# Performance work log

Hardware: AMD Instinct MI355X
Metric: run time of the kernel (lower is better)

## Reference

```python
import jax, jax.numpy as jnp
import numpy as np

NUM_GRAPHS = 128


def _gcn_layer(x, W, b, src, dst, out_norm, in_norm, n_nodes):
    # DGL GraphConv, norm='both': x * outdeg^{-1/2}, sum-aggregate src->dst, * indeg^{-1/2}, then @W + b
    x = x * out_norm[:, None]
    agg = jax.ops.segment_sum(x[src], dst, num_segments=n_nodes)  # [N, d]
    agg = agg * in_norm[:, None]
    return agg @ W + b


def setup_inputs() -> dict:
    key = jax.random.key(0)
    ks = jax.random.split(key, 10)
    N, E, D, H, P, C = 100000, 1600000, 128, 128, 64, 10
    h = jax.random.normal(ks[0], (N, D), dtype=jnp.float32)
    perm_features = jax.random.normal(ks[1], (NUM_GRAPHS, P), dtype=jnp.float32)
    W1 = jax.random.normal(ks[2], (D, H), dtype=jnp.float32) * (1.0 / np.sqrt(D))
    b1 = jnp.zeros((H,), dtype=jnp.float32)
    W2 = jax.random.normal(ks[3], (H, H), dtype=jnp.float32) * (1.0 / np.sqrt(H))
    b2 = jnp.zeros((H,), dtype=jnp.float32)
    Wc = jax.random.normal(ks[4], (H + P, C), dtype=jnp.float32) * (1.0 / np.sqrt(H + P))
    bc = jnp.zeros((C,), dtype=jnp.float32)
    src = jax.random.randint(ks[5], (E,), 0, N, dtype=jnp.int64)
    dst = jax.random.randint(ks[6], (E,), 0, N, dtype=jnp.int64)
    graph_ids = jnp.sort(jax.random.randint(ks[7], (N,), 0, NUM_GRAPHS, dtype=jnp.int64))
    return {"h": h, "perm_features": perm_features, "W1": W1, "b1": b1,
            "W2": W2, "b2": b2, "Wc": Wc, "bc": bc,
            "src": src, "dst": dst, "graph_ids": graph_ids}


def reference(h, perm_features, W1, b1, W2, b2, Wc, bc, src, dst, graph_ids):
    N = h.shape[0]
    ones_e = jnp.ones(src.shape[0], dtype=h.dtype)
    out_deg = jnp.maximum(jax.ops.segment_sum(ones_e, src, num_segments=N), 1.0)
    in_deg = jnp.maximum(jax.ops.segment_sum(ones_e, dst, num_segments=N), 1.0)
    out_norm = jax.lax.rsqrt(out_deg)
    in_norm = jax.lax.rsqrt(in_deg)

    x = _gcn_layer(h, W1, b1, src, dst, out_norm, in_norm, N)
    x = jax.nn.relu(x)
    x = _gcn_layer(x, W2, b2, src, dst, out_norm, in_norm, N)

    # dgl.mean_nodes: per-graph mean of node features
    sums = jax.ops.segment_sum(x, graph_ids, num_segments=NUM_GRAPHS)  # [G, H]
    counts = jnp.maximum(
        jax.ops.segment_sum(jnp.ones(N, dtype=x.dtype), graph_ids, num_segments=NUM_GRAPHS), 1.0)
    hg = sums / counts[:, None]

    combined = jnp.concatenate([hg, perm_features], axis=1)  # [G, H+P]
    return combined @ Wc + bc
```

## Files before the change

kernel.cpp:

```cpp
#include <hip/hip_runtime.h>


#define NUM_G 128
#define PB_EDGES 4096
#define W_BIN 128

typedef unsigned int uint32;
typedef short bf16x8 __attribute__((ext_vector_type(8)));
typedef float f32x4 __attribute__((ext_vector_type(4)));

__device__ __forceinline__ float bflo(uint32 u) { return __uint_as_float(u << 16); }
__device__ __forceinline__ float bfhi(uint32 u) { return __uint_as_float(u & 0xffff0000u); }
__device__ __forceinline__ uint32 f2bf_bits(float f) {
    uint32 b = __float_as_uint(f);
    return (b + 0x7fffu + ((b >> 16) & 1u)) >> 16;
}
__device__ __forceinline__ uint32 pack2(float a, float b) {
    return f2bf_bits(a) | (f2bf_bits(b) << 16);
}

__global__ __launch_bounds__(256) void p1_hist(const int* __restrict__ src,
                                               const int* __restrict__ dst, int E,
                                               int NBIN, int B, int* __restrict__ bh) {
    __shared__ int hist[1024];
    int b = blockIdx.x;
    int pipe = (b >= B) ? 1 : 0;
    int bb = pipe ? b - B : b;
    const int* key = pipe ? src : dst;
    for (int i = threadIdx.x; i < NBIN; i += 256) hist[i] = 0;
    __syncthreads();
    int base = bb * PB_EDGES;
    for (int c = threadIdx.x; c < PB_EDGES / 4; c += 256) {
        int e = base + c * 4;
        if (e + 3 < E) {
            int4 k4 = *(const int4*)(key + e);
            atomicAdd(&hist[k4.x >> 7], 1);
            atomicAdd(&hist[k4.y >> 7], 1);
            atomicAdd(&hist[k4.z >> 7], 1);
            atomicAdd(&hist[k4.w >> 7], 1);
        } else {
            for (int i = e; i < E && i < e + 4; i++) atomicAdd(&hist[key[i] >> 7], 1);
        }
    }
    __syncthreads();
    int* outp = bh + (size_t)pipe * NBIN * B;
    for (int k = threadIdx.x; k < NBIN; k += 256)
        outp[(size_t)k * B + bb] = hist[k];
}

__global__ __launch_bounds__(256) void p2a_tot(const int* __restrict__ bh, int NBIN, int B,
                                               int* __restrict__ tot) {
    __shared__ int sc[256];
    int k = blockIdx.x % NBIN, pipe = blockIdx.x / NBIN;
    const int* row = bh + (size_t)pipe * NBIN * B + (size_t)k * B;
    int acc = 0;
    for (int b = threadIdx.x; b < B; b += 256) acc += row[b];
    sc[threadIdx.x] = acc;
    __syncthreads();
    for (int o = 128; o > 0; o >>= 1) {
        if (threadIdx.x < o) sc[threadIdx.x] += sc[threadIdx.x + o];
        __syncthreads();
    }
    if (threadIdx.x == 0) tot[pipe * NBIN + k] = sc[0];
}

__global__ __launch_bounds__(1024) void p2b_scan(const int* __restrict__ tot, int NBIN, int E,
                                                 int* __restrict__ bstart) {
    __shared__ int sc[1024];
    int pipe = blockIdx.x;
    int i = threadIdx.x;
    int v = (i < NBIN) ? tot[pipe * NBIN + i] : 0;
    sc[i] = v;
    __syncthreads();
    for (int o = 1; o < 1024; o <<= 1) {
        int t = (i >= o) ? sc[i - o] : 0;
        __syncthreads();
        sc[i] += t;
        __syncthreads();
    }
    if (i < NBIN) bstart[pipe * (NBIN + 1) + i] = sc[i] - v;
    if (i == 0) bstart[pipe * (NBIN + 1) + NBIN] = E;
}

__global__ __launch_bounds__(512) void p2c_cursor(const int* __restrict__ bh,
                                                  const int* __restrict__ bstart,
                                                  int NBIN, int B, int* __restrict__ curs) {
    __shared__ int sc[512];
    int k = blockIdx.x % NBIN, pipe = blockIdx.x / NBIN;
    const int* row = bh + (size_t)pipe * NBIN * B + (size_t)k * B;
    int i = threadIdx.x;
    int v = (i < B) ? row[i] : 0;
    sc[i] = v;
    __syncthreads();
    for (int o = 1; o < 512; o <<= 1) {
        int t = (i >= o) ? sc[i - o] : 0;
        __syncthreads();
        sc[i] += t;
        __syncthreads();
    }
    int base = bstart[pipe * (NBIN + 1) + k];
    if (i < B)
        curs[(size_t)pipe * B * NBIN + (size_t)i * NBIN + k] = base + sc[i] - v;
}

__global__ __launch_bounds__(256) void p3_scatter(const int* __restrict__ src,
                                                  const int* __restrict__ dst, int E,
                                                  int NBIN, int B, const int* __restrict__ curs,
                                                  int2* __restrict__ ebuf, int* __restrict__ sbuf) {
    __shared__ int cur[1024];
    int b = blockIdx.x;
    int pipe = (b >= B) ? 1 : 0;
    int bb = pipe ? b - B : b;
    const int* crow = curs + (size_t)pipe * B * NBIN + (size_t)bb * NBIN;
    for (int i = threadIdx.x; i < NBIN; i += 256) cur[i] = crow[i];
    __syncthreads();
    int base = bb * PB_EDGES;
    if (!pipe) {
        for (int c = threadIdx.x; c < PB_EDGES / 4; c += 256) {
            int e = base + c * 4;
            if (e + 3 < E) {
                int4 s4 = *(const int4*)(src + e);
                int4 d4 = *(const int4*)(dst + e);
                int p;
                p = atomicAdd(&cur[d4.x >> 7], 1); ebuf[p] = make_int2(s4.x, d4.x);
                p = atomicAdd(&cur[d4.y >> 7], 1); ebuf[p] = make_int2(s4.y, d4.y);
                p = atomicAdd(&cur[d4.z >> 7], 1); ebuf[p] = make_int2(s4.z, d4.z);
                p = atomicAdd(&cur[d4.w >> 7], 1); ebuf[p] = make_int2(s4.w, d4.w);
            } else {
                for (int i = e; i < E && i < e + 4; i++) {
                    int s = src[i], d = dst[i];
                    int p = atomicAdd(&cur[d >> 7], 1);
                    ebuf[p] = make_int2(s, d);
                }
            }
        }
    } else {
        for (int c = threadIdx.x; c < PB_EDGES / 4; c += 256) {
            int e = base + c * 4;
            if (e + 3 < E) {
                int4 s4 = *(const int4*)(src + e);
                int p;
                p = atomicAdd(&cur[s4.x >> 7], 1); sbuf[p] = s4.x;
                p = atomicAdd(&cur[s4.y >> 7], 1); sbuf[p] = s4.y;
                p = atomicAdd(&cur[s4.z >> 7], 1); sbuf[p] = s4.z;
                p = atomicAdd(&cur[s4.w >> 7], 1); sbuf[p] = s4.w;
            } else {
                for (int i = e; i < E && i < e + 4; i++) {
                    int s = src[i];
                    int p = atomicAdd(&cur[s >> 7], 1);
                    sbuf[p] = s;
                }
            }
        }
    }
}

__global__ __launch_bounds__(256) void p4_csr(const int2* __restrict__ ebuf,
                                              const int* __restrict__ bstart,
                                              int NBIN, int N, int E,
                                              int* __restrict__ indeg, int* __restrict__ coff,
                                              int* __restrict__ adj) {
    __shared__ int hist[128];
    __shared__ int sc[128];
    __shared__ int cur[128];
    __shared__ int lsrc[4096];
    int k = blockIdx.x;
    int tid = threadIdx.x;
    int s0 = bstart[k], s1 = bstart[k + 1];
    int M = s1 - s0;
    if (tid < 128) hist[tid] = 0;
    __syncthreads();
    for (int i = tid; i < M; i += 256) {
        int2 e = ebuf[s0 + i];
        atomicAdd(&hist[e.y & 127], 1);
    }
    __syncthreads();
    if (tid < 128) sc[tid] = hist[tid];
    __syncthreads();
    for (int o = 1; o < 128; o <<= 1) {
        int v = 0;
        if (tid < 128 && tid >= o) v = sc[tid - o];
        __syncthreads();
        if (tid < 128) sc[tid] += v;
        __syncthreads();
    }
    if (tid < 128) {
        int node = k * W_BIN + tid;
        if (node < N) {
            indeg[node] = hist[tid];
            coff[node] = s0 + sc[tid] - hist[tid];
        }
        cur[tid] = sc[tid] - hist[tid];
    }
    if (k == NBIN - 1 && tid == 0) coff[N] = E;
    __syncthreads();
    if (M <= 4096) {
        for (int i = tid; i < M; i += 256) {
            int2 e = ebuf[s0 + i];
            int p = atomicAdd(&cur[e.y & 127], 1);
            lsrc[p] = e.x;
        }
        __syncthreads();
        for (int i = tid; i < M; i += 256) adj[s0 + i] = lsrc[i];
    } else {
        for (int i = tid; i < M; i += 256) {
            int2 e = ebuf[s0 + i];
            int p = atomicAdd(&cur[e.y & 127], 1);
            adj[s0 + p] = e.x;
        }
    }
}

__global__ __launch_bounds__(256) void p4s_outdeg(const int* __restrict__ sbuf,
                                                  const int* __restrict__ bstartS,
                                                  int N, int* __restrict__ outdeg) {
    __shared__ int hist[128];
    int k = blockIdx.x;
    int tid = threadIdx.x;
    int s0 = bstartS[k], s1 = bstartS[k + 1];
    if (tid < 128) hist[tid] = 0;
    __syncthreads();
    for (int i = s0 + tid; i < s1; i += 256) atomicAdd(&hist[sbuf[i] & 127], 1);
    __syncthreads();
    if (tid < 128) {
        int node = k * W_BIN + tid;
        if (node < N) outdeg[node] = hist[tid];
    }
}

__global__ void goffs_kernel(const int* __restrict__ gids, int N, int* __restrict__ goffs) {
    int i = blockIdx.x * blockDim.x + threadIdx.x;
    if (i > N) return;
    int prev = (i == 0) ? -1 : gids[i - 1];
    int cur  = (i == N) ? NUM_G : gids[i];
    for (int g = prev + 1; g <= cur && g <= NUM_G; g++) goffs[g] = i;
}

__global__ void norm_kernel(const int* __restrict__ outdeg, const int* __restrict__ indeg,
                            float* __restrict__ nrm_out, float* __restrict__ nrm_in, int N) {
    int i = blockIdx.x * blockDim.x + threadIdx.x;
    if (i >= N) return;
    nrm_out[i] = rsqrtf(fmaxf((float)outdeg[i], 1.0f));
    nrm_in[i]  = rsqrtf(fmaxf((float)indeg[i], 1.0f));
}

__global__ void wt_prep(const float* __restrict__ W1, const float* __restrict__ W2,
                        unsigned short* __restrict__ Wt1, unsigned short* __restrict__ Wt2) {
    int tid = blockIdx.x * blockDim.x + threadIdx.x;
    int sel = tid >> 14;
    int idx = tid & 16383;
    int k = idx >> 7, n = idx & 127;
    float v = (sel ? W2 : W1)[idx];
    unsigned short* o = sel ? Wt2 : Wt1;
    o[n * 128 + k] = (unsigned short)f2bf_bits(v);
}

__global__ void scale_kernel(const float* __restrict__ h, const float* __restrict__ nrm_out,
                             uint32* __restrict__ xsb, int N) {
    int t = blockIdx.x * blockDim.x + threadIdx.x;
    int node = t >> 4, q = t & 15;
    if (node >= N) return;
    float ns = nrm_out[node];
    const float4* hv = (const float4*)(h + (size_t)node * 128 + q * 8);
    float4 a = hv[0], b = hv[1];
    a.x *= ns; a.y *= ns; a.z *= ns; a.w *= ns;
    b.x *= ns; b.y *= ns; b.z *= ns; b.w *= ns;
    uint4 o;
    o.x = pack2(a.x, a.y); o.y = pack2(a.z, a.w);
    o.z = pack2(b.x, b.y); o.w = pack2(b.z, b.w);
    ((uint4*)xsb)[(size_t)node * 16 + q] = o;
}

__global__ void agg_kernel(const uint32* __restrict__ xsb, const int* __restrict__ adj,
                           const int* __restrict__ coff, uint32* __restrict__ aggb, int N) {
    int t = blockIdx.x * blockDim.x + threadIdx.x;
    int node = t >> 4;
    int q = t & 15;
    if (node >= N) return;
    int jb = coff[node], je = coff[node + 1];
    float acc[8];
#pragma unroll
    for (int i = 0; i < 8; i++) acc[i] = 0.f;
    for (int j = jb; j < je; j++) {
        int s = adj[j];
        uint4 u = ((const uint4*)xsb)[(size_t)s * 16 + q];
        acc[0] += bflo(u.x); acc[1] += bfhi(u.x);
        acc[2] += bflo(u.y); acc[3] += bfhi(u.y);
        acc[4] += bflo(u.z); acc[5] += bfhi(u.z);
        acc[6] += bflo(u.w); acc[7] += bfhi(u.w);
    }
    uint4 o;
    o.x = pack2(acc[0], acc[1]); o.y = pack2(acc[2], acc[3]);
    o.z = pack2(acc[4], acc[5]); o.w = pack2(acc[6], acc[7]);
    ((uint4*)aggb)[(size_t)node * 16 + q] = o;
}

__global__ __launch_bounds__(256) void gemm_mfma(const unsigned short* __restrict__ A,
                                                 const unsigned short* __restrict__ Wtg,
                                                 const float* __restrict__ bias,
                                                 const float* __restrict__ rowscale,
                                                 const float* __restrict__ postscale,
                                                 unsigned short* __restrict__ out,
                                                 int N, int do_relu) {
    __shared__ unsigned short Wl[128 * 136];
    for (int i = threadIdx.x; i < 2048; i += 256) {
        uint4 v = ((const uint4*)Wtg)[i];
        *(uint4*)&Wl[(i >> 4) * 136 + (i & 15) * 8] = v;
    }
    __syncthreads();

    int lane = threadIdx.x & 63;
    int wv = threadIdx.x >> 6;
    int col_l = lane & 15;
    int quad = lane >> 4;
    int r0w = blockIdx.x * 64 + wv * 16;
    if (r0w >= N) return;

    int arow = r0w + col_l;
    if (arow >= N) arow = N - 1;
    const unsigned short* Arow = A + (size_t)arow * 128;

    f32x4 acc[8];
#pragma unroll
    for (int t = 0; t < 8; t++) { acc[t][0] = 0.f; acc[t][1] = 0.f; acc[t][2] = 0.f; acc[t][3] = 0.f; }

#pragma unroll
    for (int kk = 0; kk < 4; kk++) {
        bf16x8 a = *(const bf16x8*)(Arow + kk * 32 + quad * 8);
        const unsigned short* wb = &Wl[(size_t)col_l * 136 + kk * 32 + quad * 8];
#pragma unroll
        for (int t = 0; t < 8; t++) {
            bf16x8 b = *(const bf16x8*)(wb + (size_t)t * 16 * 136);
            acc[t] = __builtin_amdgcn_mfma_f32_16x16x32_bf16(a, b, acc[t], 0, 0, 0);
        }
    }

    float s[4], p[4];
#pragma unroll
    for (int j = 0; j < 4; j++) {
        int rw = r0w + quad * 4 + j;
        bool ok = rw < N;
        s[j] = ok ? rowscale[rw] : 0.f;
        p[j] = (postscale != nullptr && ok) ? postscale[rw] : 1.f;
    }
#pragma unroll
    for (int t = 0; t < 8; t++) {
        int c = t * 16 + col_l;
        float bia = bias[c];
#pragma unroll
        for (int j = 0; j < 4; j++) {
            int rw = r0w + quad * 4 + j;
            if (rw >= N) continue;
            float v = fmaf(s[j], acc[t][j], bia);
            if (do_relu) v = fmaxf(v, 0.f);
            v *= p[j];
            out[(size_t)rw * 128 + c] = (unsigned short)f2bf_bits(v);
        }
    }
}

__global__ __launch_bounds__(1024) void mean_kernel(const uint32* __restrict__ x2b,
                                                    const int* __restrict__ goffs,
                                                    float* __restrict__ hg) {
    __shared__ float red[16][128];
    int g = blockIdx.x;
    int cp = threadIdx.x & 63;
    int j = threadIdx.x >> 6;
    int s = goffs[g], e = goffs[g + 1];
    float a0 = 0.f, a1 = 0.f;
    for (int r = s + j; r < e; r += 16) {
        uint32 u = x2b[(size_t)r * 64 + cp];
        a0 += bflo(u); a1 += bfhi(u);
    }
    red[j][cp * 2] = a0;
    red[j][cp * 2 + 1] = a1;
    __syncthreads();
    if (j == 0) {
        float t0 = 0.f, t1 = 0.f;
#pragma unroll
        for (int jj = 0; jj < 16; jj++) { t0 += red[jj][cp * 2]; t1 += red[jj][cp * 2 + 1]; }
        float cnt = fmaxf((float)(e - s), 1.0f);
        hg[g * 128 + cp * 2] = t0 / cnt;
        hg[g * 128 + cp * 2 + 1] = t1 / cnt;
    }
}

__global__ void final_kernel(const float* __restrict__ hg, const float* __restrict__ perm,
                             const float* __restrict__ Wc, const float* __restrict__ bc,
                             float* __restrict__ out, int G) {
    int t = blockIdx.x * blockDim.x + threadIdx.x;
    if (t >= G * 10) return;
    int g = t / 10, c = t % 10;
    float acc = bc[c];
    const float* hrow = hg + g * 128;
#pragma unroll 8
    for (int k = 0; k < 128; k++) acc = fmaf(hrow[k], Wc[k * 10 + c], acc);
    const float* prow = perm + g * 64;
#pragma unroll 8
    for (int p = 0; p < 64; p++) acc = fmaf(prow[p], Wc[(128 + p) * 10 + c], acc);
    out[t] = acc;
}

extern "C" void kernel_launch(void* const* d_in, const int* in_sizes, int n_in,
                              void* d_out, int out_size, void* d_ws, size_t ws_size,
                              hipStream_t stream) {
    const float* h    = (const float*)d_in[0];
    const float* perm = (const float*)d_in[1];
    const float* W1   = (const float*)d_in[2];
    const float* b1   = (const float*)d_in[3];
    const float* W2   = (const float*)d_in[4];
    const float* b2   = (const float*)d_in[5];
    const float* Wc   = (const float*)d_in[6];
    const float* bc   = (const float*)d_in[7];
    const int* src    = (const int*)d_in[8];
    const int* dst    = (const int*)d_in[9];
    const int* gids   = (const int*)d_in[10];
    float* out = (float*)d_out;

    const int N = in_sizes[0] / 128;
    const int E = in_sizes[8];
    const int G = NUM_G, H = 128;
    const int B = (E + PB_EDGES - 1) / PB_EDGES;
    const int NBIN = (N + W_BIN - 1) / W_BIN;

    char* w = (char*)d_ws;
    size_t off = 0;
    auto alloc = [&](size_t bytes) -> void* {
        void* p = w + off;
        off = (off + bytes + 255) & ~(size_t)255;
        return p;
    };
    uint32* xsb   = (uint32*)alloc((size_t)N * H * 2);
    uint32* aggb  = (uint32*)alloc((size_t)N * H * 2);
    uint32* x1b   = (uint32*)alloc((size_t)N * H * 2);
    unsigned short* Wt1 = (unsigned short*)alloc(16384 * 2);
    unsigned short* Wt2 = (unsigned short*)alloc(16384 * 2);
    int*    adj     = (int*)alloc((size_t)E * 4);
    int*    coff    = (int*)alloc((size_t)(N + 1) * 4);
    int*    indeg   = (int*)alloc((size_t)N * 4);
    int*    outdeg  = (int*)alloc((size_t)N * 4);
    float*  nrm_out = (float*)alloc((size_t)N * 4);
    float*  nrm_in  = (float*)alloc((size_t)N * 4);
    int*    goffs   = (int*)alloc((size_t)(G + 1) * 4);
    float*  hg      = (float*)alloc((size_t)G * H * 4);

    char* tmp = (char*)aggb;
    size_t toff = 0;
    auto talloc = [&](size_t bytes) -> void* {
        void* p = tmp + toff;
        toff = (toff + bytes + 255) & ~(size_t)255;
        return p;
    };
    int2* ebuf   = (int2*)talloc((size_t)E * 8);
    int*  sbuf   = (int*)talloc((size_t)E * 4);
    int*  bh     = (int*)talloc((size_t)2 * B * NBIN * 4);
    int*  curs   = (int*)talloc((size_t)2 * B * NBIN * 4);
    int*  tot    = (int*)talloc((size_t)2 * NBIN * 4);
    int*  bstart = (int*)talloc((size_t)2 * (NBIN + 1) * 4);

    wt_prep<<<128, 256, 0, stream>>>(W1, W2, Wt1, Wt2);

    p1_hist<<<2 * B, 256, 0, stream>>>(src, dst, E, NBIN, B, bh);
    p2a_tot<<<2 * NBIN, 256, 0, stream>>>(bh, NBIN, B, tot);
    p2b_scan<<<2, 1024, 0, stream>>>(tot, NBIN, E, bstart);
    p2c_cursor<<<2 * NBIN, 512, 0, stream>>>(bh, bstart, NBIN, B, curs);
    p3_scatter<<<2 * B, 256, 0, stream>>>(src, dst, E, NBIN, B, curs, ebuf, sbuf);
    p4_csr<<<NBIN, 256, 0, stream>>>(ebuf, bstart, NBIN, N, E, indeg, coff, adj);
    p4s_outdeg<<<NBIN, 256, 0, stream>>>(sbuf, bstart + (NBIN + 1), N, outdeg);

    goffs_kernel<<<(N + 1 + 255) / 256, 256, 0, stream>>>(gids, N, goffs);
    norm_kernel<<<(N + 255) / 256, 256, 0, stream>>>(outdeg, indeg, nrm_out, nrm_in, N);

    scale_kernel<<<(N * 16 + 255) / 256, 256, 0, stream>>>(h, nrm_out, xsb, N);
    agg_kernel<<<(N * 16 + 255) / 256, 256, 0, stream>>>(xsb, adj, coff, aggb, N);
    gemm_mfma<<<(N + 63) / 64, 256, 0, stream>>>((const unsigned short*)aggb, Wt1, b1,
                                                 nrm_in, nrm_out,
                                                 (unsigned short*)x1b, N, 1);

    agg_kernel<<<(N * 16 + 255) / 256, 256, 0, stream>>>(x1b, adj, coff, aggb, N);
    gemm_mfma<<<(N + 63) / 64, 256, 0, stream>>>((const unsigned short*)aggb, Wt2, b2,
                                                 nrm_in, nullptr,
                                                 (unsigned short*)xsb, N, 0);

    mean_kernel<<<G, 1024, 0, stream>>>(xsb, goffs, hg);
    final_kernel<<<(G * 10 + 255) / 256, 256, 0, stream>>>(hg, perm, Wc, bc, out, G);
}
```

Measured before the change: 396.7 us.

## Fuse small setup kernels, unroll aggregation gather, and double GEMM rows per wave

Several ideas are combined. The bin-offset scan is folded into the cursor kernel, and the in-degree and out-degree kernels become one launch. The goffs, norm and weight-prep kernels merge into one, and the mean and final classifier merge into one. Together these remove several launches and small round-trips through memory. The aggregation loop is unrolled by four so more row gathers are in flight, and the MFMA GEMM now computes 32 rows per wave, reusing each B fragment for two row tiles. The cost is more registers in the GEMM and redundant prefix sums in every cursor block.

```diff
diff --git a/kernel.cpp b/kernel.cpp
--- a/kernel.cpp
+++ b/kernel.cpp
@@ -64,31 +64,29 @@
     if (threadIdx.x == 0) tot[pipe * NBIN + k] = sc[0];
 }
 
-__global__ __launch_bounds__(1024) void p2b_scan(const int* __restrict__ tot, int NBIN, int E,
-                                                 int* __restrict__ bstart) {
-    __shared__ int sc[1024];
-    int pipe = blockIdx.x;
-    int i = threadIdx.x;
-    int v = (i < NBIN) ? tot[pipe * NBIN + i] : 0;
-    sc[i] = v;
-    __syncthreads();
-    for (int o = 1; o < 1024; o <<= 1) {
-        int t = (i >= o) ? sc[i - o] : 0;
-        __syncthreads();
-        sc[i] += t;
-        __syncthreads();
-    }
-    if (i < NBIN) bstart[pipe * (NBIN + 1) + i] = sc[i] - v;
-    if (i == 0) bstart[pipe * (NBIN + 1) + NBIN] = E;
-}
-
 __global__ __launch_bounds__(512) void p2c_cursor(const int* __restrict__ bh,
-                                                  const int* __restrict__ bstart,
-                                                  int NBIN, int B, int* __restrict__ curs) {
+                                                  const int* __restrict__ tot,
+                                                  int NBIN, int B, int E,
+                                                  int* __restrict__ bstart,
+                                                  int* __restrict__ curs) {
     __shared__ int sc[512];
     int k = blockIdx.x % NBIN, pipe = blockIdx.x / NBIN;
+    int i = threadIdx.x;
+    int pacc = 0;
+    for (int kk = i; kk < k; kk += 512) pacc += tot[pipe * NBIN + kk];
+    sc[i] = pacc;
+    __syncthreads();
+    for (int o = 256; o > 0; o >>= 1) {
+        if (i < o) sc[i] += sc[i + o];
+        __syncthreads();
+    }
+    int base = sc[0];
+    __syncthreads();
+    if (i == 0) {
+        bstart[pipe * (NBIN + 1) + k] = base;
+        if (k == 0) bstart[pipe * (NBIN + 1) + NBIN] = E;
+    }
     const int* row = bh + (size_t)pipe * NBIN * B + (size_t)k * B;
-    int i = threadIdx.x;
     int v = (i < B) ? row[i] : 0;
     sc[i] = v;
     __syncthreads();
@@ -98,7 +96,6 @@
         sc[i] += t;
         __syncthreads();
     }
-    int base = bstart[pipe * (NBIN + 1) + k];
     if (i < B)
         curs[(size_t)pipe * B * NBIN + (size_t)i * NBIN + k] = base + sc[i] - v;
 }
@@ -155,17 +152,33 @@
     }
 }
 
-__global__ __launch_bounds__(256) void p4_csr(const int2* __restrict__ ebuf,
-                                              const int* __restrict__ bstart,
-                                              int NBIN, int N, int E,
-                                              int* __restrict__ indeg, int* __restrict__ coff,
-                                              int* __restrict__ adj) {
+__global__ __launch_bounds__(256) void p4_comb(const int2* __restrict__ ebuf,
+                                               const int* __restrict__ sbuf,
+                                               const int* __restrict__ bstart,
+                                               int NBIN, int N, int E,
+                                               int* __restrict__ indeg, int* __restrict__ coff,
+                                               int* __restrict__ adj, int* __restrict__ outdeg) {
     __shared__ int hist[128];
     __shared__ int sc[128];
     __shared__ int cur[128];
     __shared__ int lsrc[4096];
-    int k = blockIdx.x;
+    int kb = blockIdx.x;
     int tid = threadIdx.x;
+    if (kb >= NBIN) {
+        int k = kb - NBIN;
+        const int* bstartS = bstart + (NBIN + 1);
+        int s0 = bstartS[k], s1 = bstartS[k + 1];
+        if (tid < 128) hist[tid] = 0;
+        __syncthreads();
+        for (int i = s0 + tid; i < s1; i += 256) atomicAdd(&hist[sbuf[i] & 127], 1);
+        __syncthreads();
+        if (tid < 128) {
+            int node = k * W_BIN + tid;
+            if (node < N) outdeg[node] = hist[tid];
+        }
+        return;
+    }
+    int k = kb;
     int s0 = bstart[k], s1 = bstart[k + 1];
     int M = s1 - s0;
     if (tid < 128) hist[tid] = 0;
@@ -211,48 +224,29 @@
     }
 }
 
-__global__ __launch_bounds__(256) void p4s_outdeg(const int* __restrict__ sbuf,
-                                                  const int* __restrict__ bstartS,
-                                                  int N, int* __restrict__ outdeg) {
-    __shared__ int hist[128];
-    int k = blockIdx.x;
-    int tid = threadIdx.x;
-    int s0 = bstartS[k], s1 = bstartS[k + 1];
-    if (tid < 128) hist[tid] = 0;
-    __syncthreads();
-    for (int i = s0 + tid; i < s1; i += 256) atomicAdd(&hist[sbuf[i] & 127], 1);
-    __syncthreads();
-    if (tid < 128) {
-        int node = k * W_BIN + tid;
-        if (node < N) outdeg[node] = hist[tid];
-    }
-}
-
-__global__ void goffs_kernel(const int* __restrict__ gids, int N, int* __restrict__ goffs) {
+__global__ void misc_kernel(const int* __restrict__ gids,
+                            const int* __restrict__ outdeg, const int* __restrict__ indeg,
+                            const float* __restrict__ W1, const float* __restrict__ W2,
+                            int N, int* __restrict__ goffs,
+                            float* __restrict__ nrm_out, float* __restrict__ nrm_in,
+                            unsigned short* __restrict__ Wt1, unsigned short* __restrict__ Wt2) {
     int i = blockIdx.x * blockDim.x + threadIdx.x;
-    if (i > N) return;
-    int prev = (i == 0) ? -1 : gids[i - 1];
-    int cur  = (i == N) ? NUM_G : gids[i];
-    for (int g = prev + 1; g <= cur && g <= NUM_G; g++) goffs[g] = i;
-}
-
-__global__ void norm_kernel(const int* __restrict__ outdeg, const int* __restrict__ indeg,
-                            float* __restrict__ nrm_out, float* __restrict__ nrm_in, int N) {
-    int i = blockIdx.x * blockDim.x + threadIdx.x;
-    if (i >= N) return;
-    nrm_out[i] = rsqrtf(fmaxf((float)outdeg[i], 1.0f));
-    nrm_in[i]  = rsqrtf(fmaxf((float)indeg[i], 1.0f));
-}
-
-__global__ void wt_prep(const float* __restrict__ W1, const float* __restrict__ W2,
-                        unsigned short* __restrict__ Wt1, unsigned short* __restrict__ Wt2) {
-    int tid = blockIdx.x * blockDim.x + threadIdx.x;
-    int sel = tid >> 14;
-    int idx = tid & 16383;
-    int k = idx >> 7, n = idx & 127;
-    float v = (sel ? W2 : W1)[idx];
-    unsigned short* o = sel ? Wt2 : Wt1;
-    o[n * 128 + k] = (unsigned short)f2bf_bits(v);
+    if (i <= N) {
+        int prev = (i == 0) ? -1 : gids[i - 1];
+        int cur = (i == N) ? NUM_G : gids[i];
+        for (int g = prev + 1; g <= cur && g <= NUM_G; g++) goffs[g] = i;
+    }
+    if (i < N) {
+        nrm_out[i] = rsqrtf(fmaxf((float)outdeg[i], 1.0f));
+        nrm_in[i]  = rsqrtf(fmaxf((float)indeg[i], 1.0f));
+    }
+    if (i < 32768) {
+        int sel = i >> 14;
+        int idx = i & 16383;
+        int k = idx >> 7, n = idx & 127;
+        float v = (sel ? W2 : W1)[idx];
+        (sel ? Wt2 : Wt1)[n * 128 + k] = (unsigned short)f2bf_bits(v);
+    }
 }
 
 __global__ void scale_kernel(const float* __restrict__ h, const float* __restrict__ nrm_out,
@@ -281,13 +275,28 @@
     float acc[8];
 #pragma unroll
     for (int i = 0; i < 8; i++) acc[i] = 0.f;
-    for (int j = jb; j < je; j++) {
+    const uint4* rows = (const uint4*)xsb;
+    int j = jb;
+    for (; j + 3 < je; j += 4) {
+        int s0 = adj[j], s1 = adj[j + 1], s2 = adj[j + 2], s3 = adj[j + 3];
+        uint4 u0 = rows[(size_t)s0 * 16 + q];
+        uint4 u1 = rows[(size_t)s1 * 16 + q];
+        uint4 u2 = rows[(size_t)s2 * 16 + q];
+        uint4 u3 = rows[(size_t)s3 * 16 + q];
+        acc[0] += bflo(u0.x); acc[1] += bfhi(u0.x); acc[2] += bflo(u0.y); acc[3] += bfhi(u0.y);
+        acc[4] += bflo(u0.z); acc[5] += bfhi(u0.z); acc[6] += bflo(u0.w); acc[7] += bfhi(u0.w);
+        acc[0] += bflo(u1.x); acc[1] += bfhi(u1.x); acc[2] += bflo(u1.y); acc[3] += bfhi(u1.y);
+        acc[4] += bflo(u1.z); acc[5] += bfhi(u1.z); acc[6] += bflo(u1.w); acc[7] += bfhi(u1.w);
+        acc[0] += bflo(u2.x); acc[1] += bfhi(u2.x); acc[2] += bflo(u2.y); acc[3] += bfhi(u2.y);
+        acc[4] += bflo(u2.z); acc[5] += bfhi(u2.z); acc[6] += bflo(u2.w); acc[7] += bfhi(u2.w);
+        acc[0] += bflo(u3.x); acc[1] += bfhi(u3.x); acc[2] += bflo(u3.y); acc[3] += bfhi(u3.y);
+        acc[4] += bflo(u3.z); acc[5] += bfhi(u3.z); acc[6] += bflo(u3.w); acc[7] += bfhi(u3.w);
+    }
+    for (; j < je; j++) {
         int s = adj[j];
-        uint4 u = ((const uint4*)xsb)[(size_t)s * 16 + q];
-        acc[0] += bflo(u.x); acc[1] += bfhi(u.x);
-        acc[2] += bflo(u.y); acc[3] += bfhi(u.y);
-        acc[4] += bflo(u.z); acc[5] += bfhi(u.z);
-        acc[6] += bflo(u.w); acc[7] += bfhi(u.w);
+        uint4 u = rows[(size_t)s * 16 + q];
+        acc[0] += bflo(u.x); acc[1] += bfhi(u.x); acc[2] += bflo(u.y); acc[3] += bfhi(u.y);
+        acc[4] += bflo(u.z); acc[5] += bfhi(u.z); acc[6] += bflo(u.w); acc[7] += bfhi(u.w);
     }
     uint4 o;
     o.x = pack2(acc[0], acc[1]); o.y = pack2(acc[2], acc[3]);
@@ -313,56 +322,72 @@
     int wv = threadIdx.x >> 6;
     int col_l = lane & 15;
     int quad = lane >> 4;
-    int r0w = blockIdx.x * 64 + wv * 16;
+    int r0w = blockIdx.x * 128 + wv * 32;
     if (r0w >= N) return;
 
-    int arow = r0w + col_l;
-    if (arow >= N) arow = N - 1;
-    const unsigned short* Arow = A + (size_t)arow * 128;
-
-    f32x4 acc[8];
-#pragma unroll
-    for (int t = 0; t < 8; t++) { acc[t][0] = 0.f; acc[t][1] = 0.f; acc[t][2] = 0.f; acc[t][3] = 0.f; }
+    int arow0 = r0w + col_l;        if (arow0 >= N) arow0 = N - 1;
+    int arow1 = r0w + 16 + col_l;   if (arow1 >= N) arow1 = N - 1;
+    const unsigned short* Ar0 = A + (size_t)arow0 * 128;
+    const unsigned short* Ar1 = A + (size_t)arow1 * 128;
+
+    f32x4 acc[2][8];
+#pragma unroll
+    for (int rt = 0; rt < 2; rt++)
+#pragma unroll
+        for (int t = 0; t < 8; t++) {
+            acc[rt][t][0] = 0.f; acc[rt][t][1] = 0.f;
+            acc[rt][t][2] = 0.f; acc[rt][t][3] = 0.f;
+        }
 
 #pragma unroll
     for (int kk = 0; kk < 4; kk++) {
-        bf16x8 a = *(const bf16x8*)(Arow + kk * 32 + quad * 8);
+        bf16x8 a0 = *(const bf16x8*)(Ar0 + kk * 32 + quad * 8);
+        bf16x8 a1 = *(const bf16x8*)(Ar1 + kk * 32 + quad * 8);
         const unsigned short* wb = &Wl[(size_t)col_l * 136 + kk * 32 + quad * 8];
 #pragma unroll
         for (int t = 0; t < 8; t++) {
             bf16x8 b = *(const bf16x8*)(wb + (size_t)t * 16 * 136);
-            acc[t] = __builtin_amdgcn_mfma_f32_16x16x32_bf16(a, b, acc[t], 0, 0, 0);
-        }
-    }
-
-    float s[4], p[4];
-#pragma unroll
-    for (int j = 0; j < 4; j++) {
-        int rw = r0w + quad * 4 + j;
-        bool ok = rw < N;
-        s[j] = ok ? rowscale[rw] : 0.f;
-        p[j] = (postscale != nullptr && ok) ? postscale[rw] : 1.f;
-    }
-#pragma unroll
-    for (int t = 0; t < 8; t++) {
-        int c = t * 16 + col_l;
-        float bia = bias[c];
+            acc[0][t] = __builtin_amdgcn_mfma_f32_16x16x32_bf16(a0, b, acc[0][t], 0, 0, 0);
+            acc[1][t] = __builtin_amdgcn_mfma_f32_16x16x32_bf16(a1, b, acc[1][t], 0, 0, 0);
+        }
+    }
+
+#pragma unroll
+    for (int rt = 0; rt < 2; rt++) {
+        int rbase = r0w + rt * 16;
+        float s[4], p[4];
 #pragma unroll
         for (int j = 0; j < 4; j++) {
-            int rw = r0w + quad * 4 + j;
-            if (rw >= N) continue;
-            float v = fmaf(s[j], acc[t][j], bia);
-            if (do_relu) v = fmaxf(v, 0.f);
-            v *= p[j];
-            out[(size_t)rw * 128 + c] = (unsigned short)f2bf_bits(v);
-        }
-    }
-}
-
-__global__ __launch_bounds__(1024) void mean_kernel(const uint32* __restrict__ x2b,
-                                                    const int* __restrict__ goffs,
-                                                    float* __restrict__ hg) {
+            int rw = rbase + quad * 4 + j;
+            bool ok = rw < N;
+            s[j] = ok ? rowscale[ok ? rw : 0] : 0.f;
+            p[j] = (postscale != nullptr && ok) ? postscale[rw] : 1.f;
+        }
+#pragma unroll
+        for (int t = 0; t < 8; t++) {
+            int c = t * 16 + col_l;
+            float bia = bias[c];
+#pragma unroll
+            for (int j = 0; j < 4; j++) {
+                int rw = rbase + quad * 4 + j;
+                if (rw >= N) continue;
+                float v = fmaf(s[j], acc[rt][t][j], bia);
+                if (do_relu) v = fmaxf(v, 0.f);
+                v *= p[j];
+                out[(size_t)rw * 128 + c] = (unsigned short)f2bf_bits(v);
+            }
+        }
+    }
+}
+
+__global__ __launch_bounds__(1024) void mean_final(const uint32* __restrict__ x2b,
+                                                   const int* __restrict__ goffs,
+                                                   const float* __restrict__ perm,
+                                                   const float* __restrict__ Wc,
+                                                   const float* __restrict__ bc,
+                                                   float* __restrict__ out) {
     __shared__ float red[16][128];
+    __shared__ float hrow[128];
     int g = blockIdx.x;
     int cp = threadIdx.x & 63;
     int j = threadIdx.x >> 6;
@@ -380,25 +405,20 @@
 #pragma unroll
         for (int jj = 0; jj < 16; jj++) { t0 += red[jj][cp * 2]; t1 += red[jj][cp * 2 + 1]; }
         float cnt = fmaxf((float)(e - s), 1.0f);
-        hg[g * 128 + cp * 2] = t0 / cnt;
-        hg[g * 128 + cp * 2 + 1] = t1 / cnt;
-    }
-}
-
-__global__ void final_kernel(const float* __restrict__ hg, const float* __restrict__ perm,
-                             const float* __restrict__ Wc, const float* __restrict__ bc,
-                             float* __restrict__ out, int G) {
-    int t = blockIdx.x * blockDim.x + threadIdx.x;
-    if (t >= G * 10) return;
-    int g = t / 10, c = t % 10;
-    float acc = bc[c];
-    const float* hrow = hg + g * 128;
+        hrow[cp * 2] = t0 / cnt;
+        hrow[cp * 2 + 1] = t1 / cnt;
+    }
+    __syncthreads();
+    if (threadIdx.x < 10) {
+        int c = threadIdx.x;
+        float acc = bc[c];
 #pragma unroll 8
-    for (int k = 0; k < 128; k++) acc = fmaf(hrow[k], Wc[k * 10 + c], acc);
-    const float* prow = perm + g * 64;
+        for (int k = 0; k < 128; k++) acc = fmaf(hrow[k], Wc[k * 10 + c], acc);
+        const float* prow = perm + g * 64;
 #pragma unroll 8
-    for (int p = 0; p < 64; p++) acc = fmaf(prow[p], Wc[(128 + p) * 10 + c], acc);
-    out[t] = acc;
+        for (int p = 0; p < 64; p++) acc = fmaf(prow[p], Wc[(128 + p) * 10 + c], acc);
+        out[g * 10 + c] = acc;
+    }
 }
 
 extern "C" void kernel_launch(void* const* d_in, const int* in_sizes, int n_in,
@@ -442,7 +462,6 @@
     float*  nrm_out = (float*)alloc((size_t)N * 4);
     float*  nrm_in  = (float*)alloc((size_t)N * 4);
     int*    goffs   = (int*)alloc((size_t)(G + 1) * 4);
-    float*  hg      = (float*)alloc((size_t)G * H * 4);
 
     char* tmp = (char*)aggb;
     size_t toff = 0;
@@ -458,30 +477,26 @@
     int*  tot    = (int*)talloc((size_t)2 * NBIN * 4);
     int*  bstart = (int*)talloc((size_t)2 * (NBIN + 1) * 4);
 
-    wt_prep<<<128, 256, 0, stream>>>(W1, W2, Wt1, Wt2);
-
     p1_hist<<<2 * B, 256, 0, stream>>>(src, dst, E, NBIN, B, bh);
     p2a_tot<<<2 * NBIN, 256, 0, stream>>>(bh, NBIN, B, tot);
-    p2b_scan<<<2, 1024, 0, stream>>>(tot, NBIN, E, bstart);
-    p2c_cursor<<<2 * NBIN, 512, 0, stream>>>(bh, bstart, NBIN, B, curs);
+    p2c_cursor<<<2 * NBIN, 512, 0, stream>>>(bh, tot, NBIN, B, E, bstart, curs);
     p3_scatter<<<2 * B, 256, 0, stream>>>(src, dst, E, NBIN, B, curs, ebuf, sbuf);
-    p4_csr<<<NBIN, 256, 0, stream>>>(ebuf, bstart, NBIN, N, E, indeg, coff, adj);
-    p4s_outdeg<<<NBIN, 256, 0, stream>>>(sbuf, bstart + (NBIN + 1), N, outdeg);
-
-    goffs_kernel<<<(N + 1 + 255) / 256, 256, 0, stream>>>(gids, N, goffs);
-    norm_kernel<<<(N + 255) / 256, 256, 0, stream>>>(outdeg, indeg, nrm_out, nrm_in, N);
+    p4_comb<<<2 * NBIN, 256, 0, stream>>>(ebuf, sbuf, bstart, NBIN, N, E,
+                                          indeg, coff, adj, outdeg);
+
+    misc_kernel<<<(N + 1 + 255) / 256, 256, 0, stream>>>(gids, outdeg, indeg, W1, W2, N,
+                                                         goffs, nrm_out, nrm_in, Wt1, Wt2);
 
     scale_kernel<<<(N * 16 + 255) / 256, 256, 0, stream>>>(h, nrm_out, xsb, N);
     agg_kernel<<<(N * 16 + 255) / 256, 256, 0, stream>>>(xsb, adj, coff, aggb, N);
-    gemm_mfma<<<(N + 63) / 64, 256, 0, stream>>>((const unsigned short*)aggb, Wt1, b1,
-                                                 nrm_in, nrm_out,
-                                                 (unsigned short*)x1b, N, 1);
+    gemm_mfma<<<(N + 127) / 128, 256, 0, stream>>>((const unsigned short*)aggb, Wt1, b1,
+                                                   nrm_in, nrm_out,
+                                                   (unsigned short*)x1b, N, 1);
 
     agg_kernel<<<(N * 16 + 255) / 256, 256, 0, stream>>>(x1b, adj, coff, aggb, N);
-    gemm_mfma<<<(N + 63) / 64, 256, 0, stream>>>((const unsigned short*)aggb, Wt2, b2,
-                                                 nrm_in, nullptr,
-                                                 (unsigned short*)xsb, N, 0);
-
-    mean_kernel<<<G, 1024, 0, stream>>>(xsb, goffs, hg);
-    final_kernel<<<(G * 10 + 255) / 256, 256, 0, stream>>>(hg, perm, Wc, bc, out, G);
-}
+    gemm_mfma<<<(N + 127) / 128, 256, 0, stream>>>((const unsigned short*)aggb, Wt2, b2,
+                                                   nrm_in, nullptr,
+                                                   (unsigned short*)xsb, N, 0);
+
+    mean_final<<<G, 1024, 0, stream>>>(xsb, goffs, perm, Wc, bc, out);
+}
```

Result: faster. 354.4 us (-10.7%).
